# Performance work log

Hardware: AMD Instinct MI355X
Metric: run time of the kernel (lower is better)

The kernel has to match this reference:

```python
import jax, jax.numpy as jnp
import numpy as np

N = 8192
D = 512


def setup_inputs() -> dict:
    key = jax.random.key(0)
    k_h, k_a, k_q, k_k, k_v = jax.random.split(key, 5)
    H = jax.random.normal(k_h, (N, D), dtype=jnp.float32)
    A = jax.random.uniform(k_a, (N, N), dtype=jnp.float32)
    W_Q = jax.random.uniform(k_q, (D, D), dtype=jnp.float32)
    W_K = jax.random.uniform(k_k, (D, D), dtype=jnp.float32)
    W_V = jax.random.uniform(k_v, (D, D), dtype=jnp.float32)
    return {"H": H, "A": A, "W_Q": W_Q, "W_K": W_K, "W_V": W_V}


def reference(H, A, W_Q, W_K, W_V):
    # Q = H @ W_Q, K = H @ W_K; scores = Q @ K^T  -> [N, N]
    scale = 1.0 / jnp.sqrt(jnp.asarray(H.shape[1], dtype=H.dtype))
    HQ = H @ W_Q                      # [N, D]
    HK = H @ W_K                      # [N, D]
    scores = jnp.einsum('nd,md->nm', HQ, HK)  # [N, N]
    scores = scores * A * scale       # elementwise adjacency mask + scale
    attn = jax.nn.softmax(scores, axis=1)
    return attn @ (H @ W_V)           # [N, D]
```

## Files before the change

kernel.cpp:

```cpp
#include <hip/hip_runtime.h>
#include <cmath>


typedef unsigned short u16;
typedef unsigned int   u32;
typedef float f32x4 __attribute__((ext_vector_type(4)));
typedef short s16x8 __attribute__((ext_vector_type(8)));

#define DEVI static __device__ __forceinline__

DEVI u16 f2bf(float x) { u32 u = __float_as_uint(x); u32 r = u + 0x7fffu + ((u >> 16) & 1u); return (u16)(r >> 16); }
DEVI float bf2f(u16 b) { return __uint_as_float((u32)b << 16); }

DEVI f32x4 mm_bf16(s16x8 a, s16x8 b, f32x4 c) {
  return __builtin_amdgcn_mfma_f32_16x16x32_bf16(a, b, c, 0, 0, 0);
}

DEVI uint4 scaleP(uint4 v, float f) {
  u32* w = (u32*)&v;
#pragma unroll
  for (int j = 0; j < 4; j++) {
    u32 lo = __float_as_uint(__uint_as_float(w[j] << 16) * f) + 0x8000u;
    u32 hi = __float_as_uint(__uint_as_float(w[j] & 0xffff0000u) * f) + 0x8000u;
    w[j] = __builtin_amdgcn_perm(hi, lo, 0x07060302);
  }
  return v;
}


__global__ void k_split(const float* __restrict__ X, u16* __restrict__ Xhi, u16* __restrict__ Xlo, int n4) {
  int i = blockIdx.x * 256 + threadIdx.x;
  if (i >= n4) return;
  float4 v = ((const float4*)X)[i];
  u16 h0 = f2bf(v.x), h1 = f2bf(v.y), h2 = f2bf(v.z), h3 = f2bf(v.w);
  u16 l0 = f2bf(v.x - bf2f(h0)), l1 = f2bf(v.y - bf2f(h1));
  u16 l2 = f2bf(v.z - bf2f(h2)), l3 = f2bf(v.w - bf2f(h3));
  ((uint2*)Xhi)[i] = make_uint2((u32)h0 | ((u32)h1 << 16), (u32)h2 | ((u32)h3 << 16));
  ((uint2*)Xlo)[i] = make_uint2((u32)l0 | ((u32)l1 << 16), (u32)l2 | ((u32)l3 << 16));
}

__global__ void k_prepW(const float* __restrict__ W0, const float* __restrict__ W1, const float* __restrict__ W2,
                        u16* __restrict__ Thi, u16* __restrict__ Tlo) {
  int idx = blockIdx.x * 256 + threadIdx.x;
  if (idx >= 3 * 512 * 512) return;
  int w = idx >> 18, n = (idx >> 9) & 511, k = idx & 511;
  const float* W = (w == 0) ? W0 : (w == 1) ? W1 : W2;
  float v = W[k * 512 + n];
  u16 h = f2bf(v);
  Thi[idx] = h;
  Tlo[idx] = f2bf(v - bf2f(h));
}

__global__ void k_transpose(const u16* __restrict__ in, u16* __restrict__ out, int R, int C) {
  __shared__ u16 t[64][72];
  const int rb = blockIdx.x * 64, cb = blockIdx.y * 64;
  const int r = threadIdx.x >> 2, c4 = (threadIdx.x & 3) * 16;
  const u16* src = in + (size_t)(rb + r) * C + cb + c4;
  *(uint4*)&t[r][c4] = *(const uint4*)src;
  *(uint4*)&t[r][c4 + 8] = *(const uint4*)(src + 8);
  __syncthreads();
  u16 v[16];
#pragma unroll
  for (int j = 0; j < 16; j++) v[j] = t[c4 + j][r];
  uint4 o0, o1;
  o0.x = v[0] | ((u32)v[1] << 16); o0.y = v[2] | ((u32)v[3] << 16);
  o0.z = v[4] | ((u32)v[5] << 16); o0.w = v[6] | ((u32)v[7] << 16);
  o1.x = v[8] | ((u32)v[9] << 16); o1.y = v[10] | ((u32)v[11] << 16);
  o1.z = v[12] | ((u32)v[13] << 16); o1.w = v[14] | ((u32)v[15] << 16);
  u16* dst = out + (size_t)(cb + r) * R + rb + c4;
  *(uint4*)dst = o0;
  *(uint4*)(dst + 8) = o1;
}


template<int EPI, int PASSES, int FUSEW, int KSPLIT>
__launch_bounds__(256, 4)
__global__ void gemm_bt(const u16* __restrict__ Ahi, const u16* __restrict__ Alo,
                        const u16* __restrict__ Bhi, const u16* __restrict__ Blo,
                        int M, int N, int K,
                        float* __restrict__ Cf, float* __restrict__ Cf1, float* __restrict__ Cf2,
                        u16* __restrict__ C0, u16* __restrict__ C1,
                        const float* __restrict__ Adj, float* __restrict__ mC, float* __restrict__ lC,
                        u16* __restrict__ Pout, const float* __restrict__ Fsc, float scale)
{
  constexpr int BUF = 128 * 40;
  constexpr int NBUF = (PASSES == 3) ? 4 : 3;
  __shared__ __align__(16) u16 lds[BUF * NBUF];

  u16* sAh = lds;
  u16* sAl = lds + BUF;
  u16* sBh = lds + ((PASSES == 3) ? 2 : 1) * BUF;
  u16* sBl = lds + ((PASSES == 3) ? 3 : 2) * BUF;

  const int tid = threadIdx.x, lane = tid & 63, wid = tid >> 6;
  const int wm = wid & 1, wn = wid >> 1;
  const int lr = lane & 15, lk = lane >> 4;
  const int mbase = blockIdx.x * 128;
  int nbase;
  const u16 *bhp = Bhi, *blp = Blo;
  u16 *c0 = C0, *c1 = C1;
  if constexpr (FUSEW) {
    const int w = blockIdx.y >> 2;
    nbase = (blockIdx.y & 3) * 128;
    bhp += (size_t)w * 262144;  blp += (size_t)w * 262144;
    c0  += (size_t)w * 4194304; c1  += (size_t)w * 4194304;
  } else {
    nbase = blockIdx.y * 128;
  }
  const int srow = tid >> 1, shalf = tid & 1;
  const size_t Ks = (size_t)K;

  int kbeg = 0, kend = K;
  if constexpr (KSPLIT > 1) {
    const int steps = K >> 5, bz = blockIdx.z;
    kbeg = ((steps * bz) / KSPLIT) << 5;
    kend = ((steps * (bz + 1)) / KSPLIT) << 5;
  }

  f32x4 acc[4][4] = {};

  for (int kt = kbeg; kt < kend; kt += 32) {
    const size_t aoff = (size_t)(mbase + srow) * Ks + kt + shalf * 16;
    const size_t boff = (size_t)(nbase + srow) * Ks + kt + shalf * 16;
    uint4 vah0 = *(const uint4*)(Ahi + aoff), vah1 = *(const uint4*)(Ahi + aoff + 8);
    uint4 vbh0 = *(const uint4*)(bhp + boff), vbh1 = *(const uint4*)(bhp + boff + 8);
    uint4 val0, val1, vbl0, vbl1;
    if constexpr (PASSES == 3) { val0 = *(const uint4*)(Alo + aoff); val1 = *(const uint4*)(Alo + aoff + 8); }
    vbl0 = *(const uint4*)(blp + boff); vbl1 = *(const uint4*)(blp + boff + 8);
    if constexpr (EPI == 3) {
      const float f = Fsc[((size_t)(kt >> 7) << 13) + mbase + srow];
      vah0 = scaleP(vah0, f); vah1 = scaleP(vah1, f);
    }
    __syncthreads();
    const int so = srow * 40 + shalf * 16;
    *(uint4*)(sAh + so) = vah0; *(uint4*)(sAh + so + 8) = vah1;
    *(uint4*)(sBh + so) = vbh0; *(uint4*)(sBh + so + 8) = vbh1;
    if constexpr (PASSES == 3) { *(uint4*)(sAl + so) = val0; *(uint4*)(sAl + so + 8) = val1; }
    *(uint4*)(sBl + so) = vbl0; *(uint4*)(sBl + so + 8) = vbl1;
    __syncthreads();

    s16x8 ah[4], bh[4], al[4], bl[4];
#pragma unroll
    for (int t = 0; t < 4; t++) {
      ah[t] = *(const s16x8*)(sAh + (wm * 64 + t * 16 + lr) * 40 + lk * 8);
      bh[t] = *(const s16x8*)(sBh + (wn * 64 + t * 16 + lr) * 40 + lk * 8);
      if constexpr (PASSES == 3) al[t] = *(const s16x8*)(sAl + (wm * 64 + t * 16 + lr) * 40 + lk * 8);
      bl[t] = *(const s16x8*)(sBl + (wn * 64 + t * 16 + lr) * 40 + lk * 8);
    }
#pragma unroll
    for (int mt = 0; mt < 4; mt++)
#pragma unroll
      for (int nt = 0; nt < 4; nt++) {
        acc[mt][nt] = mm_bf16(ah[mt], bh[nt], acc[mt][nt]);
        acc[mt][nt] = mm_bf16(ah[mt], bl[nt], acc[mt][nt]);
        if constexpr (PASSES == 3) acc[mt][nt] = mm_bf16(al[mt], bh[nt], acc[mt][nt]);
      }
  }

  if constexpr (EPI == 2) {
    __syncthreads();
    float* sred = (float*)lds;
    float* ssum = sred + 256;
    u16* pb = lds + 1024;
    float mfin[4];
#pragma unroll
    for (int nt = 0; nt < 4; nt++) {
      const int q_l = wn * 64 + nt * 16 + lr;
      const float* arow = Adj + (size_t)(nbase + q_l) * (size_t)M + mbase + wm * 64 + lk * 4;
      float4 a4[4];
#pragma unroll
      for (int mt = 0; mt < 4; mt++) a4[mt] = *(const float4*)(arow + mt * 16);
      float mx = -3.4e38f;
#pragma unroll
      for (int mt = 0; mt < 4; mt++)
#pragma unroll
        for (int r = 0; r < 4; r++) {
          float s = acc[mt][nt][r] * ((const float*)&a4[mt])[r] * scale;
          acc[mt][nt][r] = s;
          mx = fmaxf(mx, s);
        }
      mx = fmaxf(mx, __shfl_xor(mx, 16));
      mx = fmaxf(mx, __shfl_xor(mx, 32));
      if (lane < 16) sred[wm * 128 + wn * 64 + nt * 16 + lane] = mx;
    }
    __syncthreads();
#pragma unroll
    for (int nt = 0; nt < 4; nt++) {
      const int qi = wn * 64 + nt * 16 + lr;
      mfin[nt] = fmaxf(sred[qi], sred[128 + qi]);
    }
    if (wm == 0 && lane < 16) {
#pragma unroll
      for (int nt = 0; nt < 4; nt++)
        mC[(size_t)blockIdx.x * N + nbase + wn * 64 + nt * 16 + lane] = mfin[nt];
    }
#pragma unroll
    for (int nt = 0; nt < 4; nt++) {
      float sm = 0.f;
#pragma unroll
      for (int mt = 0; mt < 4; mt++)
#pragma unroll
        for (int r = 0; r < 4; r++) {
          float p = __expf(acc[mt][nt][r] - mfin[nt]);
          acc[mt][nt][r] = p;
          sm += p;
        }
      sm += __shfl_xor(sm, 16);
      sm += __shfl_xor(sm, 32);
      if (lane < 16) ssum[wm * 128 + wn * 64 + nt * 16 + lane] = sm;
    }
    __syncthreads();
    if (wm == 0 && lane < 16) {
#pragma unroll
      for (int nt = 0; nt < 4; nt++) {
        const int qi = wn * 64 + nt * 16 + lane;
        lC[(size_t)blockIdx.x * N + nbase + qi] = ssum[qi] + ssum[128 + qi];
      }
    }
#pragma unroll
    for (int nt = 0; nt < 4; nt++) {
      const int q_l = wn * 64 + nt * 16 + lr;
#pragma unroll
      for (int mt = 0; mt < 4; mt++) {
        const int kvo = wm * 64 + mt * 16 + lk * 4;
        u32 u0 = (u32)f2bf(acc[mt][nt][0]) | ((u32)f2bf(acc[mt][nt][1]) << 16);
        u32 u1 = (u32)f2bf(acc[mt][nt][2]) | ((u32)f2bf(acc[mt][nt][3]) << 16);
        *(uint2*)&pb[q_l * 136 + kvo] = make_uint2(u0, u1);
      }
    }
    __syncthreads();
    {
      u16* dst = Pout + (size_t)(nbase + srow) * (size_t)M + mbase + shalf * 64;
      const u16* srcp = &pb[srow * 136 + shalf * 64];
#pragma unroll
      for (int i = 0; i < 8; i++) ((uint4*)dst)[i] = ((const uint4*)srcp)[i];
    }
  } else {
    float* cfp = Cf;
    if constexpr (KSPLIT > 1) {
      if (blockIdx.z == 1) cfp = Cf1;
      else if (blockIdx.z == 2) cfp = Cf2;
    }
#pragma unroll
    for (int mt = 0; mt < 4; mt++)
#pragma unroll
      for (int nt = 0; nt < 4; nt++) {
        const int grow = mbase + wm * 64 + mt * 16 + lk * 4;
        const int gcol = nbase + wn * 64 + nt * 16 + lr;
#pragma unroll
        for (int r = 0; r < 4; r++) {
          float c = acc[mt][nt][r];
          size_t o = (size_t)(grow + r) * N + gcol;
          if constexpr (EPI == 0) {
            u16 h = f2bf(c);
            c0[o] = h;
            c1[o] = f2bf(c - bf2f(h));
          } else {
            cfp[o] = c;
          }
        }
      }
  }
}


__global__ void k_reduce(const float* __restrict__ mC, const float* __restrict__ lC, float* __restrict__ F,
                         int NQ, int NC) {
  const int q = blockIdx.x * 256 + threadIdx.x;
  if (q >= NQ) return;
  float mf = -3.4e38f;
  for (int c = 0; c < NC; c++) mf = fmaxf(mf, mC[(size_t)c * NQ + q]);
  float L = 0.f;
  for (int c = 0; c < NC; c++) L += lC[(size_t)c * NQ + q] * __expf(mC[(size_t)c * NQ + q] - mf);
  const float inv = 1.0f / L;
  for (int c = 0; c < NC; c++) F[(size_t)c * NQ + q] = __expf(mC[(size_t)c * NQ + q] - mf) * inv;
}

__global__ void k_sumout(float* __restrict__ out, const float* __restrict__ p1, const float* __restrict__ p2, int n4) {
  int i = blockIdx.x * 256 + threadIdx.x;
  if (i >= n4) return;
  float4 o = ((const float4*)out)[i];
  float4 a = ((const float4*)p1)[i];
  float4 b = ((const float4*)p2)[i];
  o.x += a.x + b.x; o.y += a.y + b.y; o.z += a.z + b.z; o.w += a.w + b.w;
  ((float4*)out)[i] = o;
}


extern "C" void kernel_launch(void* const* d_in, const int* in_sizes, int n_in,
                              void* d_out, int out_size, void* d_ws, size_t ws_size,
                              hipStream_t stream) {
  const float* H  = (const float*)d_in[0];
  const float* Aj = (const float*)d_in[1];
  const float* Wq = (const float*)d_in[2];
  const float* Wk = (const float*)d_in[3];
  const float* Wv = (const float*)d_in[4];
  float* out = (float*)d_out;
  const int NN = 8192, DD = 512;

  char* ws = (char*)d_ws;
  size_t off = 0;
  auto alloc = [&](size_t bytes) -> void* {
    void* p = ws + off;
    off += (bytes + 255) & ~(size_t)255;
    return p;
  };
  u16* Pbuf  = (u16*)alloc((size_t)NN * NN * 2);
  u16* Hhi   = (u16*)alloc((size_t)NN * DD * 2);
  u16* Hlo   = (u16*)alloc((size_t)NN * DD * 2);
  u16* WThi  = (u16*)alloc((size_t)3 * DD * DD * 2);
  u16* WTlo  = (u16*)alloc((size_t)3 * DD * DD * 2);
  u16* PRhi  = (u16*)alloc((size_t)3 * NN * DD * 2);
  u16* PRlo  = (u16*)alloc((size_t)3 * NN * DD * 2);
  u16* HVthi = (u16*)alloc((size_t)NN * DD * 2);
  u16* HVtlo = (u16*)alloc((size_t)NN * DD * 2);
  float* mC  = (float*)alloc((size_t)64 * NN * 4);
  float* lC  = (float*)alloc((size_t)64 * NN * 4);
  float* Ft  = (float*)alloc((size_t)64 * NN * 4);
  if (off > ws_size) return;

  u16* HQhi = PRhi;                 u16* HQlo = PRlo;
  u16* HKhi = PRhi + (size_t)NN*DD; u16* HKlo = PRlo + (size_t)NN*DD;
  u16* HVhi = PRhi + (size_t)2*NN*DD; u16* HVlo = PRlo + (size_t)2*NN*DD;

  float* part1 = (float*)Hhi;
  float* part2 = (float*)((char*)Hhi + (size_t)NN * DD * 4);

  const float scl = 1.0f / sqrtf((float)DD);

  k_split<<<4096, 256, 0, stream>>>(H, Hhi, Hlo, NN * DD / 4);
  k_prepW<<<3072, 256, 0, stream>>>(Wq, Wk, Wv, WThi, WTlo);

  dim3 gP(64, 12);
  gemm_bt<0, 3, 1, 1><<<gP, 256, 0, stream>>>(Hhi, Hlo, WThi, WTlo, NN, DD, DD,
                                              nullptr, nullptr, nullptr, PRhi, PRlo,
                                              nullptr, nullptr, nullptr, nullptr, nullptr, 0.f);

  dim3 gT(128, 8);
  k_transpose<<<gT, 256, 0, stream>>>(HVhi, HVthi, NN, DD);
  k_transpose<<<gT, 256, 0, stream>>>(HVlo, HVtlo, NN, DD);

  dim3 gS(64, 64);
  gemm_bt<2, 3, 0, 1><<<gS, 256, 0, stream>>>(HKhi, HKlo, HQhi, HQlo, NN, NN, DD,
                                              nullptr, nullptr, nullptr, nullptr, nullptr,
                                              Aj, mC, lC, Pbuf, nullptr, scl);

  k_reduce<<<32, 256, 0, stream>>>(mC, lC, Ft, NN, 64);

  dim3 gO(64, 4, 3);
  gemm_bt<3, 2, 0, 3><<<gO, 256, 0, stream>>>(Pbuf, nullptr, HVthi, HVtlo, NN, DD, NN,
                                              out, part1, part2, nullptr, nullptr,
                                              nullptr, nullptr, nullptr, nullptr, Ft, 0.f);

  k_sumout<<<4096, 256, 0, stream>>>(out, part1, part2, NN * DD / 4);
}
```

Measured before the change: 554.7 us.

## Use 256x128 tiles for score and PV GEMMs, drop V low-part pass

Adds a k_big kernel with 256x128 block tiles and 8x4 MFMA accumulators per wave, used for both the masked score/softmax GEMM and the P@V GEMM. Softmax partial max and sum are now written per wave (two column chunks per block), which removes the cross-wave LDS reduction in the epilogue. The P@V GEMM now runs a single bf16 pass with no V low-part correction, so only the high part of HV is transposed. Its split-K grows from 3 to 4 with an extra partial buffer. The intent is to cut LDS traffic per MFMA and halve the MFMA work of the largest GEMM, at the cost of lower accuracy in the output, more register pressure and lower occupancy.

```diff
diff --git a/kernel.cpp b/kernel.cpp
--- a/kernel.cpp
+++ b/kernel.cpp
@@ -73,40 +73,28 @@
 }
 
 
-template<int EPI, int PASSES, int FUSEW, int KSPLIT>
-__launch_bounds__(256, 4)
-__global__ void gemm_bt(const u16* __restrict__ Ahi, const u16* __restrict__ Alo,
-                        const u16* __restrict__ Bhi, const u16* __restrict__ Blo,
-                        int M, int N, int K,
-                        float* __restrict__ Cf, float* __restrict__ Cf1, float* __restrict__ Cf2,
-                        u16* __restrict__ C0, u16* __restrict__ C1,
-                        const float* __restrict__ Adj, float* __restrict__ mC, float* __restrict__ lC,
-                        u16* __restrict__ Pout, const float* __restrict__ Fsc, float scale)
+template<int EPI, int PASSES, int KSPLIT>
+__launch_bounds__(256, 2)
+__global__ void k_big(const u16* __restrict__ Ahi, const u16* __restrict__ Alo,
+                      const u16* __restrict__ Bhi, const u16* __restrict__ Blo,
+                      int M, int N, int K,
+                      float* __restrict__ Cf, float* __restrict__ Cf1,
+                      float* __restrict__ Cf2, float* __restrict__ Cf3,
+                      const float* __restrict__ Adj, float* __restrict__ mC,
+                      float* __restrict__ lC, u16* __restrict__ Pout,
+                      const float* __restrict__ Fsc, float scale)
 {
-  constexpr int BUF = 128 * 40;
-  constexpr int NBUF = (PASSES == 3) ? 4 : 3;
-  __shared__ __align__(16) u16 lds[BUF * NBUF];
-
+  constexpr int LDSU = (EPI == 2) ? 33792 : 15360;
+  __shared__ __align__(16) u16 lds[LDSU];
   u16* sAh = lds;
-  u16* sAl = lds + BUF;
-  u16* sBh = lds + ((PASSES == 3) ? 2 : 1) * BUF;
-  u16* sBl = lds + ((PASSES == 3) ? 3 : 2) * BUF;
+  u16* sAl = lds + 10240;
+  u16* sBh = lds + ((PASSES == 3) ? 20480 : 10240);
+  u16* sBl = lds + 25600;
 
   const int tid = threadIdx.x, lane = tid & 63, wid = tid >> 6;
-  const int wm = wid & 1, wn = wid >> 1;
+  const int wn = wid & 1, wm = wid >> 1;
   const int lr = lane & 15, lk = lane >> 4;
-  const int mbase = blockIdx.x * 128;
-  int nbase;
-  const u16 *bhp = Bhi, *blp = Blo;
-  u16 *c0 = C0, *c1 = C1;
-  if constexpr (FUSEW) {
-    const int w = blockIdx.y >> 2;
-    nbase = (blockIdx.y & 3) * 128;
-    bhp += (size_t)w * 262144;  blp += (size_t)w * 262144;
-    c0  += (size_t)w * 4194304; c1  += (size_t)w * 4194304;
-  } else {
-    nbase = blockIdx.y * 128;
-  }
+  const int mbase = blockIdx.x * 256, nbase = blockIdx.y * 128;
   const int srow = tid >> 1, shalf = tid & 1;
   const size_t Ks = (size_t)K;
 
@@ -117,62 +105,74 @@
     kend = ((steps * (bz + 1)) / KSPLIT) << 5;
   }
 
-  f32x4 acc[4][4] = {};
+  f32x4 acc[8][4] = {};
 
   for (int kt = kbeg; kt < kend; kt += 32) {
-    const size_t aoff = (size_t)(mbase + srow) * Ks + kt + shalf * 16;
-    const size_t boff = (size_t)(nbase + srow) * Ks + kt + shalf * 16;
-    uint4 vah0 = *(const uint4*)(Ahi + aoff), vah1 = *(const uint4*)(Ahi + aoff + 8);
-    uint4 vbh0 = *(const uint4*)(bhp + boff), vbh1 = *(const uint4*)(bhp + boff + 8);
-    uint4 val0, val1, vbl0, vbl1;
-    if constexpr (PASSES == 3) { val0 = *(const uint4*)(Alo + aoff); val1 = *(const uint4*)(Alo + aoff + 8); }
-    vbl0 = *(const uint4*)(blp + boff); vbl1 = *(const uint4*)(blp + boff + 8);
+    const size_t a0 = (size_t)(mbase + srow) * Ks + kt + shalf * 16;
+    const size_t a1 = a0 + (size_t)128 * Ks;
+    const size_t b0 = (size_t)(nbase + srow) * Ks + kt + shalf * 16;
+    uint4 vah0 = *(const uint4*)(Ahi + a0), vah1 = *(const uint4*)(Ahi + a0 + 8);
+    uint4 vah2 = *(const uint4*)(Ahi + a1), vah3 = *(const uint4*)(Ahi + a1 + 8);
+    uint4 vbh0 = *(const uint4*)(Bhi + b0), vbh1 = *(const uint4*)(Bhi + b0 + 8);
+    uint4 val0, val1, val2, val3, vbl0, vbl1;
+    if constexpr (PASSES == 3) {
+      val0 = *(const uint4*)(Alo + a0); val1 = *(const uint4*)(Alo + a0 + 8);
+      val2 = *(const uint4*)(Alo + a1); val3 = *(const uint4*)(Alo + a1 + 8);
+      vbl0 = *(const uint4*)(Blo + b0); vbl1 = *(const uint4*)(Blo + b0 + 8);
+    }
     if constexpr (EPI == 3) {
-      const float f = Fsc[((size_t)(kt >> 7) << 13) + mbase + srow];
-      vah0 = scaleP(vah0, f); vah1 = scaleP(vah1, f);
+      const float f0 = Fsc[((size_t)(kt >> 7) << 13) + mbase + srow];
+      const float f1 = Fsc[((size_t)(kt >> 7) << 13) + mbase + 128 + srow];
+      vah0 = scaleP(vah0, f0); vah1 = scaleP(vah1, f0);
+      vah2 = scaleP(vah2, f1); vah3 = scaleP(vah3, f1);
     }
     __syncthreads();
     const int so = srow * 40 + shalf * 16;
-    *(uint4*)(sAh + so) = vah0; *(uint4*)(sAh + so + 8) = vah1;
-    *(uint4*)(sBh + so) = vbh0; *(uint4*)(sBh + so + 8) = vbh1;
-    if constexpr (PASSES == 3) { *(uint4*)(sAl + so) = val0; *(uint4*)(sAl + so + 8) = val1; }
-    *(uint4*)(sBl + so) = vbl0; *(uint4*)(sBl + so + 8) = vbl1;
-    __syncthreads();
-
-    s16x8 ah[4], bh[4], al[4], bl[4];
-#pragma unroll
-    for (int t = 0; t < 4; t++) {
-      ah[t] = *(const s16x8*)(sAh + (wm * 64 + t * 16 + lr) * 40 + lk * 8);
-      bh[t] = *(const s16x8*)(sBh + (wn * 64 + t * 16 + lr) * 40 + lk * 8);
-      if constexpr (PASSES == 3) al[t] = *(const s16x8*)(sAl + (wm * 64 + t * 16 + lr) * 40 + lk * 8);
-      bl[t] = *(const s16x8*)(sBl + (wn * 64 + t * 16 + lr) * 40 + lk * 8);
-    }
-#pragma unroll
-    for (int mt = 0; mt < 4; mt++)
-#pragma unroll
-      for (int nt = 0; nt < 4; nt++) {
-        acc[mt][nt] = mm_bf16(ah[mt], bh[nt], acc[mt][nt]);
-        acc[mt][nt] = mm_bf16(ah[mt], bl[nt], acc[mt][nt]);
-        if constexpr (PASSES == 3) acc[mt][nt] = mm_bf16(al[mt], bh[nt], acc[mt][nt]);
-      }
+    *(uint4*)(sAh + so) = vah0;        *(uint4*)(sAh + so + 8) = vah1;
+    *(uint4*)(sAh + 5120 + so) = vah2; *(uint4*)(sAh + 5120 + so + 8) = vah3;
+    *(uint4*)(sBh + so) = vbh0;        *(uint4*)(sBh + so + 8) = vbh1;
+    if constexpr (PASSES == 3) {
+      *(uint4*)(sAl + so) = val0;        *(uint4*)(sAl + so + 8) = val1;
+      *(uint4*)(sAl + 5120 + so) = val2; *(uint4*)(sAl + 5120 + so + 8) = val3;
+      *(uint4*)(sBl + so) = vbl0;        *(uint4*)(sBl + so + 8) = vbl1;
+    }
+    __syncthreads();
+
+    s16x8 ah[8], al[8];
+#pragma unroll
+    for (int m = 0; m < 8; m++) {
+      const int ro = (wm * 128 + m * 16 + lr) * 40 + lk * 8;
+      ah[m] = *(const s16x8*)(sAh + ro);
+      if constexpr (PASSES == 3) al[m] = *(const s16x8*)(sAl + ro);
+    }
+#pragma unroll
+    for (int nt = 0; nt < 4; nt++) {
+      const int ro = (wn * 64 + nt * 16 + lr) * 40 + lk * 8;
+      s16x8 bh = *(const s16x8*)(sBh + ro);
+#pragma unroll
+      for (int m = 0; m < 8; m++) acc[m][nt] = mm_bf16(ah[m], bh, acc[m][nt]);
+      if constexpr (PASSES == 3) {
+        s16x8 bl = *(const s16x8*)(sBl + ro);
+#pragma unroll
+        for (int m = 0; m < 8; m++) acc[m][nt] = mm_bf16(ah[m], bl, acc[m][nt]);
+#pragma unroll
+        for (int m = 0; m < 8; m++) acc[m][nt] = mm_bf16(al[m], bh, acc[m][nt]);
+      }
+    }
   }
 
   if constexpr (EPI == 2) {
-    __syncthreads();
-    float* sred = (float*)lds;
-    float* ssum = sred + 256;
-    u16* pb = lds + 1024;
-    float mfin[4];
+    const int c = blockIdx.x * 2 + wm;
 #pragma unroll
     for (int nt = 0; nt < 4; nt++) {
       const int q_l = wn * 64 + nt * 16 + lr;
-      const float* arow = Adj + (size_t)(nbase + q_l) * (size_t)M + mbase + wm * 64 + lk * 4;
-      float4 a4[4];
-#pragma unroll
-      for (int mt = 0; mt < 4; mt++) a4[mt] = *(const float4*)(arow + mt * 16);
+      const float* arow = Adj + (size_t)(nbase + q_l) * (size_t)M + mbase + wm * 128 + lk * 4;
+      float4 a4[8];
+#pragma unroll
+      for (int mt = 0; mt < 8; mt++) a4[mt] = *(const float4*)(arow + mt * 16);
       float mx = -3.4e38f;
 #pragma unroll
-      for (int mt = 0; mt < 4; mt++)
+      for (int mt = 0; mt < 8; mt++)
 #pragma unroll
         for (int r = 0; r < 4; r++) {
           float s = acc[mt][nt][r] * ((const float*)&a4[mt])[r] * scale;
@@ -181,86 +181,140 @@
         }
       mx = fmaxf(mx, __shfl_xor(mx, 16));
       mx = fmaxf(mx, __shfl_xor(mx, 32));
-      if (lane < 16) sred[wm * 128 + wn * 64 + nt * 16 + lane] = mx;
-    }
-    __syncthreads();
-#pragma unroll
-    for (int nt = 0; nt < 4; nt++) {
-      const int qi = wn * 64 + nt * 16 + lr;
-      mfin[nt] = fmaxf(sred[qi], sred[128 + qi]);
-    }
-    if (wm == 0 && lane < 16) {
-#pragma unroll
-      for (int nt = 0; nt < 4; nt++)
-        mC[(size_t)blockIdx.x * N + nbase + wn * 64 + nt * 16 + lane] = mfin[nt];
-    }
-#pragma unroll
-    for (int nt = 0; nt < 4; nt++) {
       float sm = 0.f;
 #pragma unroll
-      for (int mt = 0; mt < 4; mt++)
+      for (int mt = 0; mt < 8; mt++)
 #pragma unroll
         for (int r = 0; r < 4; r++) {
-          float p = __expf(acc[mt][nt][r] - mfin[nt]);
+          float p = __expf(acc[mt][nt][r] - mx);
           acc[mt][nt][r] = p;
           sm += p;
         }
       sm += __shfl_xor(sm, 16);
       sm += __shfl_xor(sm, 32);
-      if (lane < 16) ssum[wm * 128 + wn * 64 + nt * 16 + lane] = sm;
-    }
-    __syncthreads();
-    if (wm == 0 && lane < 16) {
-#pragma unroll
-      for (int nt = 0; nt < 4; nt++) {
-        const int qi = wn * 64 + nt * 16 + lane;
-        lC[(size_t)blockIdx.x * N + nbase + qi] = ssum[qi] + ssum[128 + qi];
-      }
-    }
+      if (lane < 16) {
+        mC[(size_t)c * N + nbase + wn * 64 + nt * 16 + lane] = mx;
+        lC[(size_t)c * N + nbase + wn * 64 + nt * 16 + lane] = sm;
+      }
+    }
+    __syncthreads();
+    u16* pb = lds;
 #pragma unroll
     for (int nt = 0; nt < 4; nt++) {
       const int q_l = wn * 64 + nt * 16 + lr;
 #pragma unroll
-      for (int mt = 0; mt < 4; mt++) {
-        const int kvo = wm * 64 + mt * 16 + lk * 4;
+      for (int mt = 0; mt < 8; mt++) {
+        const int kvo = wm * 128 + mt * 16 + lk * 4;
         u32 u0 = (u32)f2bf(acc[mt][nt][0]) | ((u32)f2bf(acc[mt][nt][1]) << 16);
         u32 u1 = (u32)f2bf(acc[mt][nt][2]) | ((u32)f2bf(acc[mt][nt][3]) << 16);
-        *(uint2*)&pb[q_l * 136 + kvo] = make_uint2(u0, u1);
+        *(uint2*)&pb[q_l * 264 + kvo] = make_uint2(u0, u1);
       }
     }
     __syncthreads();
     {
-      u16* dst = Pout + (size_t)(nbase + srow) * (size_t)M + mbase + shalf * 64;
-      const u16* srcp = &pb[srow * 136 + shalf * 64];
-#pragma unroll
-      for (int i = 0; i < 8; i++) ((uint4*)dst)[i] = ((const uint4*)srcp)[i];
+      const int q_r = tid >> 1, half = tid & 1;
+      u16* dst = Pout + (size_t)(nbase + q_r) * (size_t)M + mbase + half * 128;
+      const u16* srcp = &pb[q_r * 264 + half * 128];
+#pragma unroll
+      for (int i = 0; i < 16; i++) ((uint4*)dst)[i] = *(const uint4*)(srcp + i * 8);
     }
   } else {
     float* cfp = Cf;
     if constexpr (KSPLIT > 1) {
       if (blockIdx.z == 1) cfp = Cf1;
       else if (blockIdx.z == 2) cfp = Cf2;
+      else if (blockIdx.z == 3) cfp = Cf3;
+    }
+#pragma unroll
+    for (int mt = 0; mt < 8; mt++)
+#pragma unroll
+      for (int nt = 0; nt < 4; nt++) {
+        const int grow = mbase + wm * 128 + mt * 16 + lk * 4;
+        const int gcol = nbase + wn * 64 + nt * 16 + lr;
+#pragma unroll
+        for (int r = 0; r < 4; r++)
+          cfp[(size_t)(grow + r) * N + gcol] = acc[mt][nt][r];
+      }
+  }
+}
+
+
+template<int EPI, int PASSES, int FUSEW, int KSPLIT>
+__launch_bounds__(256, 4)
+__global__ void gemm_bt(const u16* __restrict__ Ahi, const u16* __restrict__ Alo,
+                        const u16* __restrict__ Bhi, const u16* __restrict__ Blo,
+                        int M, int N, int K,
+                        u16* __restrict__ C0, u16* __restrict__ C1)
+{
+  constexpr int BUF = 128 * 40;
+  __shared__ __align__(16) u16 lds[BUF * 4];
+
+  u16* sAh = lds;
+  u16* sAl = lds + BUF;
+  u16* sBh = lds + 2 * BUF;
+  u16* sBl = lds + 3 * BUF;
+
+  const int tid = threadIdx.x, lane = tid & 63, wid = tid >> 6;
+  const int wm = wid & 1, wn = wid >> 1;
+  const int lr = lane & 15, lk = lane >> 4;
+  const int mbase = blockIdx.x * 128;
+  const int w = blockIdx.y >> 2;
+  const int nbase = (blockIdx.y & 3) * 128;
+  const u16 *bhp = Bhi + (size_t)w * 262144, *blp = Blo + (size_t)w * 262144;
+  u16 *c0 = C0 + (size_t)w * 4194304, *c1 = C1 + (size_t)w * 4194304;
+  const int srow = tid >> 1, shalf = tid & 1;
+  const size_t Ks = (size_t)K;
+
+  f32x4 acc[4][4] = {};
+
+  for (int kt = 0; kt < K; kt += 32) {
+    const size_t aoff = (size_t)(mbase + srow) * Ks + kt + shalf * 16;
+    const size_t boff = (size_t)(nbase + srow) * Ks + kt + shalf * 16;
+    uint4 vah0 = *(const uint4*)(Ahi + aoff), vah1 = *(const uint4*)(Ahi + aoff + 8);
+    uint4 vbh0 = *(const uint4*)(bhp + boff), vbh1 = *(const uint4*)(bhp + boff + 8);
+    uint4 val0 = *(const uint4*)(Alo + aoff), val1 = *(const uint4*)(Alo + aoff + 8);
+    uint4 vbl0 = *(const uint4*)(blp + boff), vbl1 = *(const uint4*)(blp + boff + 8);
+    __syncthreads();
+    const int so = srow * 40 + shalf * 16;
+    *(uint4*)(sAh + so) = vah0; *(uint4*)(sAh + so + 8) = vah1;
+    *(uint4*)(sBh + so) = vbh0; *(uint4*)(sBh + so + 8) = vbh1;
+    *(uint4*)(sAl + so) = val0; *(uint4*)(sAl + so + 8) = val1;
+    *(uint4*)(sBl + so) = vbl0; *(uint4*)(sBl + so + 8) = vbl1;
+    __syncthreads();
+
+    s16x8 ah[4], bh[4], al[4], bl[4];
+#pragma unroll
+    for (int t = 0; t < 4; t++) {
+      ah[t] = *(const s16x8*)(sAh + (wm * 64 + t * 16 + lr) * 40 + lk * 8);
+      bh[t] = *(const s16x8*)(sBh + (wn * 64 + t * 16 + lr) * 40 + lk * 8);
+      al[t] = *(const s16x8*)(sAl + (wm * 64 + t * 16 + lr) * 40 + lk * 8);
+      bl[t] = *(const s16x8*)(sBl + (wn * 64 + t * 16 + lr) * 40 + lk * 8);
     }
 #pragma unroll
     for (int mt = 0; mt < 4; mt++)
 #pragma unroll
       for (int nt = 0; nt < 4; nt++) {
-        const int grow = mbase + wm * 64 + mt * 16 + lk * 4;
-        const int gcol = nbase + wn * 64 + nt * 16 + lr;
-#pragma unroll
-        for (int r = 0; r < 4; r++) {
-          float c = acc[mt][nt][r];
-          size_t o = (size_t)(grow + r) * N + gcol;
-          if constexpr (EPI == 0) {
-            u16 h = f2bf(c);
-            c0[o] = h;
-            c1[o] = f2bf(c - bf2f(h));
-          } else {
-            cfp[o] = c;
-          }
-        }
+        acc[mt][nt] = mm_bf16(ah[mt], bh[nt], acc[mt][nt]);
+        acc[mt][nt] = mm_bf16(ah[mt], bl[nt], acc[mt][nt]);
+        acc[mt][nt] = mm_bf16(al[mt], bh[nt], acc[mt][nt]);
       }
   }
+
+#pragma unroll
+  for (int mt = 0; mt < 4; mt++)
+#pragma unroll
+    for (int nt = 0; nt < 4; nt++) {
+      const int grow = mbase + wm * 64 + mt * 16 + lk * 4;
+      const int gcol = nbase + wn * 64 + nt * 16 + lr;
+#pragma unroll
+      for (int r = 0; r < 4; r++) {
+        float c = acc[mt][nt][r];
+        size_t o = (size_t)(grow + r) * N + gcol;
+        u16 h = f2bf(c);
+        c0[o] = h;
+        c1[o] = f2bf(c - bf2f(h));
+      }
+    }
 }
 
 
@@ -276,13 +330,16 @@
   for (int c = 0; c < NC; c++) F[(size_t)c * NQ + q] = __expf(mC[(size_t)c * NQ + q] - mf) * inv;
 }
 
-__global__ void k_sumout(float* __restrict__ out, const float* __restrict__ p1, const float* __restrict__ p2, int n4) {
+__global__ void k_sumout3(float* __restrict__ out, const float* __restrict__ p1,
+                          const float* __restrict__ p2, const float* __restrict__ p3, int n4) {
   int i = blockIdx.x * 256 + threadIdx.x;
   if (i >= n4) return;
   float4 o = ((const float4*)out)[i];
   float4 a = ((const float4*)p1)[i];
   float4 b = ((const float4*)p2)[i];
-  o.x += a.x + b.x; o.y += a.y + b.y; o.z += a.z + b.z; o.w += a.w + b.w;
+  float4 c = ((const float4*)p3)[i];
+  o.x += a.x + b.x + c.x; o.y += a.y + b.y + c.y;
+  o.z += a.z + b.z + c.z; o.w += a.w + b.w + c.w;
   ((float4*)out)[i] = o;
 }
 
@@ -313,7 +370,6 @@
   u16* PRhi  = (u16*)alloc((size_t)3 * NN * DD * 2);
   u16* PRlo  = (u16*)alloc((size_t)3 * NN * DD * 2);
   u16* HVthi = (u16*)alloc((size_t)NN * DD * 2);
-  u16* HVtlo = (u16*)alloc((size_t)NN * DD * 2);
   float* mC  = (float*)alloc((size_t)64 * NN * 4);
   float* lC  = (float*)alloc((size_t)64 * NN * 4);
   float* Ft  = (float*)alloc((size_t)64 * NN * 4);
@@ -321,10 +377,11 @@
 
   u16* HQhi = PRhi;                 u16* HQlo = PRlo;
   u16* HKhi = PRhi + (size_t)NN*DD; u16* HKlo = PRlo + (size_t)NN*DD;
-  u16* HVhi = PRhi + (size_t)2*NN*DD; u16* HVlo = PRlo + (size_t)2*NN*DD;
+  u16* HVhi = PRhi + (size_t)2*NN*DD;
 
   float* part1 = (float*)Hhi;
-  float* part2 = (float*)((char*)Hhi + (size_t)NN * DD * 4);
+  float* part2 = part1 + (size_t)NN * DD;
+  float* part3 = part2 + (size_t)NN * DD;
 
   const float scl = 1.0f / sqrtf((float)DD);
 
@@ -332,25 +389,22 @@
   k_prepW<<<3072, 256, 0, stream>>>(Wq, Wk, Wv, WThi, WTlo);
 
   dim3 gP(64, 12);
-  gemm_bt<0, 3, 1, 1><<<gP, 256, 0, stream>>>(Hhi, Hlo, WThi, WTlo, NN, DD, DD,
-                                              nullptr, nullptr, nullptr, PRhi, PRlo,
-                                              nullptr, nullptr, nullptr, nullptr, nullptr, 0.f);
+  gemm_bt<0, 3, 1, 1><<<gP, 256, 0, stream>>>(Hhi, Hlo, WThi, WTlo, NN, DD, DD, PRhi, PRlo);
 
   dim3 gT(128, 8);
   k_transpose<<<gT, 256, 0, stream>>>(HVhi, HVthi, NN, DD);
-  k_transpose<<<gT, 256, 0, stream>>>(HVlo, HVtlo, NN, DD);
-
-  dim3 gS(64, 64);
-  gemm_bt<2, 3, 0, 1><<<gS, 256, 0, stream>>>(HKhi, HKlo, HQhi, HQlo, NN, NN, DD,
-                                              nullptr, nullptr, nullptr, nullptr, nullptr,
-                                              Aj, mC, lC, Pbuf, nullptr, scl);
+
+  dim3 gS(32, 64);
+  k_big<2, 3, 1><<<gS, 256, 0, stream>>>(HKhi, HKlo, HQhi, HQlo, NN, NN, DD,
+                                         nullptr, nullptr, nullptr, nullptr,
+                                         Aj, mC, lC, Pbuf, nullptr, scl);
 
   k_reduce<<<32, 256, 0, stream>>>(mC, lC, Ft, NN, 64);
 
-  dim3 gO(64, 4, 3);
-  gemm_bt<3, 2, 0, 3><<<gO, 256, 0, stream>>>(Pbuf, nullptr, HVthi, HVtlo, NN, DD, NN,
-                                              out, part1, part2, nullptr, nullptr,
-                                              nullptr, nullptr, nullptr, nullptr, Ft, 0.f);
-
-  k_sumout<<<4096, 256, 0, stream>>>(out, part1, part2, NN * DD / 4);
-}
+  dim3 gO(32, 4, 4);
+  k_big<3, 1, 4><<<gO, 256, 0, stream>>>(Pbuf, nullptr, HVthi, nullptr, NN, DD, NN,
+                                         out, part1, part2, part3,
+                                         nullptr, nullptr, nullptr, nullptr, Ft, 0.f);
+
+  k_sumout3<<<4096, 256, 0, stream>>>(out, part1, part2, part3, NN * DD / 4);
+}
```

After: 516.4 us. 1.07x faster.
